# Performance work log

Hardware: AMD Instinct MI355X
Metric: run time of the kernel (lower is better)

Reference implementation:

```python
import jax, jax.numpy as jnp
import numpy as np

N_E = 16384
E_DIM = 256
SRC_DIM = 1024
BETA = 0.25


def setup_inputs() -> dict:
    key = jax.random.key(0)
    k_x, k_ew, k_eb, k_cb, k_dw, k_db = jax.random.split(key, 6)
    x = jax.random.normal(k_x, (16, 576, SRC_DIM), dtype=jnp.float32)
    # encoder Linear(source_dim -> embed_dim)
    enc_w = jax.random.normal(k_ew, (SRC_DIM, E_DIM), dtype=jnp.float32) / np.sqrt(SRC_DIM)
    enc_b = jax.random.normal(k_eb, (E_DIM,), dtype=jnp.float32) * 0.01
    # codebook initialized uniform(-1/n_e, 1/n_e) as in the torch module
    codebook = jax.random.uniform(k_cb, (N_E, E_DIM), dtype=jnp.float32, minval=-1.0 / N_E, maxval=1.0 / N_E)
    # decoder Linear(embed_dim -> source_dim)
    dec_w = jax.random.normal(k_dw, (E_DIM, SRC_DIM), dtype=jnp.float32) / np.sqrt(E_DIM)
    dec_b = jax.random.normal(k_db, (SRC_DIM,), dtype=jnp.float32) * 0.01
    return {"x": x, "enc_w": enc_w, "enc_b": enc_b, "codebook": codebook, "dec_w": dec_w, "dec_b": dec_b}


def reference(x, enc_w, enc_b, codebook, dec_w, dec_b):
    # encode: [B,S,src] -> [B,S,e]
    z = jnp.einsum('bsd,de->bse', x, enc_w) + enc_b
    # squared distances to all codebook entries: ||z||^2 + ||E||^2 - 2 z.E^T
    z2 = jnp.sum(z * z, axis=-1, keepdims=True)            # [B,S,1]
    e2 = jnp.sum(codebook * codebook, axis=-1)             # [n_e]
    cross = jnp.einsum('bse,ne->bsn', z, codebook)         # [B,S,n_e]
    d = z2 + e2 - 2.0 * cross
    idx = jnp.argmin(d, axis=-1)                           # [B,S] int
    z_q = codebook[idx]                                    # [B,S,e]
    sg = jax.lax.stop_gradient
    loss = BETA * jnp.mean((sg(z_q) - z) ** 2) + jnp.mean((z_q - sg(z)) ** 2)
    z_q_st = z + sg(z_q - z)                               # straight-through
    out = jnp.einsum('bse,ed->bsd', z_q_st, dec_w) + dec_b
    return (out, loss)
```

## Files before the change

kernel.cpp:

```cpp
#include <hip/hip_runtime.h>

typedef __bf16 bf16;
typedef __bf16 bf16x8 __attribute__((ext_vector_type(8)));
typedef float f32x4 __attribute__((ext_vector_type(4)));
typedef int i32x8 __attribute__((ext_vector_type(8)));
typedef unsigned int u32;
typedef unsigned char u8;

#define N_TOK 9216
#define SRC 1024
#define EDIM 256
#define NE 16384
#define GROUPS 16
#define GSIZE 1024
#define NBLK_GATHER 2304
#define NEG_CB_SCALE -8192.0f
#define E2_SCALE 4096.0f
#define LOSS_DENOM 2359296.0f

__device__ __forceinline__ void async_load16(const void* g, void* l) {
  __builtin_amdgcn_global_load_lds(
      (__attribute__((address_space(1))) void*)(void*)(const_cast<void*>(g)),
      (__attribute__((address_space(3))) void*)l, 16, 0, 0);
}

__device__ __forceinline__ f32x4 mfma16(bf16x8 a, bf16x8 b, f32x4 c) {
  return __builtin_amdgcn_mfma_f32_16x16x32_bf16(a, b, c, 0, 0, 0);
}
__device__ __forceinline__ f32x4 mfma_mx(i32x8 a, i32x8 b, f32x4 c) {
  return __builtin_amdgcn_mfma_scale_f32_16x16x128_f8f6f4(
      a, b, c, 0, 0, 0, 0x7F7F7F7F, 0, 0x7F7F7F7F);
}

__global__ __launch_bounds__(256) void k_prep(const float* __restrict__ enc_w,
                                              const float* __restrict__ dec_w,
                                              const float* __restrict__ cb,
                                              bf16* __restrict__ enc_wT,
                                              bf16* __restrict__ dec_wT,
                                              u32* __restrict__ cbb8,
                                              float* __restrict__ e2s) {
  int b = blockIdx.x;
  if (b < 1024) {
    int id = b * 256 + threadIdx.x;
    {
      int n = id >> 10, k = id & 1023;
      enc_wT[id] = (bf16)enc_w[k * EDIM + n];
    }
    {
      int n = id >> 8, k = id & 255;
      dec_wT[id] = (bf16)dec_w[k * SRC + n];
    }
  } else {
    int row = (b - 1024) * 4 + (threadIdx.x >> 6);
    int lane = threadIdx.x & 63;
    int slot = lane >> 2;
    int h = (slot & 8) | ((slot & 7) ^ (row & 7));
    int k0 = h * 16 + (lane & 3) * 4;
    float4 v = *(const float4*)(cb + (size_t)row * EDIM + k0);
    int pk = __builtin_amdgcn_cvt_pk_fp8_f32(v.x * NEG_CB_SCALE, v.y * NEG_CB_SCALE, 0, false);
    pk = __builtin_amdgcn_cvt_pk_fp8_f32(v.z * NEG_CB_SCALE, v.w * NEG_CB_SCALE, pk, true);
    cbb8[(size_t)row * 64 + lane] = (u32)pk;
    float sq = v.x * v.x + v.y * v.y + v.z * v.z + v.w * v.w;
#pragma unroll
    for (int off = 32; off; off >>= 1) sq += __shfl_xor(sq, off, 64);
    if (lane == 0) e2s[row] = E2_SCALE * (sq + 1.0f);
  }
}

__global__ __launch_bounds__(256) void k_enc(const float* __restrict__ x,
                                             const bf16* __restrict__ wT,
                                             const float* __restrict__ bias,
                                             u8* __restrict__ z8) {
  __shared__ __align__(16) bf16 As[2][64 * 32];
  __shared__ __align__(16) bf16 Bs[2][128 * 32];
  const int tid = threadIdx.x;
  const int wid = tid >> 6, lane = tid & 63;
  const int col = lane & 15, quad = lane >> 4;
  const int wm = (wid >> 1) * 32, wn = (wid & 1) * 64;
  const int bm = blockIdx.x * 64, bn = blockIdx.y * 128;
  f32x4 acc[2][4] = {};
  const int arow = tid >> 2, ags = tid & 3;

  float4 q0, q1;
  auto loadA = [&](int kc) {
    const float* p = x + (size_t)(bm + arow) * SRC + kc + ags * 8;
    q0 = *(const float4*)p;
    q1 = *(const float4*)(p + 4);
  };
  auto writeA = [&](int bb) {
    bf16x8 o = {(bf16)q0.x, (bf16)q0.y, (bf16)q0.z, (bf16)q0.w,
                (bf16)q1.x, (bf16)q1.y, (bf16)q1.z, (bf16)q1.w};
    *(bf16x8*)((char*)&As[bb][0] + (arow * 4 + (ags ^ (arow & 3))) * 16) = o;
  };
  auto stageB = [&](int kc, int bb) {
#pragma unroll
    for (int j = 0; j < 2; j++) {
      int slot = wid * 128 + j * 64 + lane;
      int row = slot >> 2;
      int gg = (slot & 3) ^ (row & 3);
      async_load16(wT + (size_t)(bn + row) * SRC + kc + gg * 8,
                   (char*)&Bs[bb][0] + wid * 2048 + j * 1024);
    }
  };

  loadA(0);
  writeA(0);
  stageB(0, 0);
  for (int it = 0; it < 32; it++) {
    int cbuf = it & 1, nbuf = cbuf ^ 1;
    if (it < 31) loadA((it + 1) * 32);
    __syncthreads();
    if (it < 31) stageB((it + 1) * 32, nbuf);
    bf16x8 afr[2], bfr[4];
#pragma unroll
    for (int t = 0; t < 2; t++) {
      int row = wm + t * 16 + col;
      afr[t] = *(const bf16x8*)((const char*)&As[cbuf][0] +
                                (row * 4 + (quad ^ (row & 3))) * 16);
    }
#pragma unroll
    for (int u = 0; u < 4; u++) {
      int row = wn + u * 16 + col;
      bfr[u] = *(const bf16x8*)((const char*)&Bs[cbuf][0] +
                                (row * 4 + (quad ^ (row & 3))) * 16);
    }
#pragma unroll
    for (int t = 0; t < 2; t++)
#pragma unroll
      for (int u = 0; u < 4; u++) acc[t][u] = mfma16(afr[t], bfr[u], acc[t][u]);
    if (it < 31) writeA(nbuf);
  }
#pragma unroll
  for (int u = 0; u < 4; u++) {
    int n = bn + wn + u * 16 + col;
    float bv = bias[n];
#pragma unroll
    for (int t = 0; t < 2; t++)
#pragma unroll
      for (int r = 0; r < 4; r++) {
        int m = bm + wm + t * 16 + quad * 4 + r;
        float v = acc[t][u][r] + bv;
        int pk = __builtin_amdgcn_cvt_pk_fp8_f32(v, v, 0, false);
        z8[(size_t)m * EDIM + n] = (u8)(pk & 0xFF);
      }
  }
}

__global__ __launch_bounds__(256, 3) void k_argmin(const u8* __restrict__ zb8,
                                                   const u8* __restrict__ cbb8,
                                                   const float* __restrict__ e2s,
                                                   float* __restrict__ pval,
                                                   int* __restrict__ pidx) {
  __shared__ __align__(16) u8 Cs[2 * 16384];
  const int tid = threadIdx.x;
  const int wid = tid >> 6, lane = tid & 63;
  const int col = lane & 15, quad = lane >> 4;
  const int g = blockIdx.y;
  const int tw = blockIdx.x * 192 + wid * 48;

  i32x8 af[3][2];
#pragma unroll
  for (int t = 0; t < 3; t++)
#pragma unroll
    for (int m = 0; m < 2; m++) {
      const u8* p = zb8 + (size_t)(tw + t * 16 + col) * EDIM + m * 128 + quad * 32;
      int4 lo = *(const int4*)p;
      int4 hi = *(const int4*)(p + 16);
      af[t][m] = (i32x8){lo.x, lo.y, lo.z, lo.w, hi.x, hi.y, hi.z, hi.w};
    }

  u32 best[3][4];
#pragma unroll
  for (int t = 0; t < 3; t++)
#pragma unroll
    for (int r = 0; r < 4; r++) best[t][r] = 0xFFFFFFFFu;

  auto stage_load = [&](int st, int bb) {
    const u8* src = cbb8 + (size_t)(g * GSIZE + st * 64) * EDIM;
#pragma unroll
    for (int j = 0; j < 4; j++) {
      async_load16(src + (wid * 256 + j * 64 + lane) * 16,
                   (char*)Cs + bb * 16384 + wid * 4096 + j * 1024);
    }
  };

  auto compute = [&](int st, int bb) {
    const char* bbase = (const char*)Cs + bb * 16384;
    const int cb0 = g * GSIZE + st * 64;
    float ev[4];
#pragma unroll
    for (int u = 0; u < 4; u++) ev[u] = e2s[cb0 + u * 16 + col];
    f32x4 c[3][4] = {};
    const int r7 = col & 7;
#pragma unroll
    for (int m = 0; m < 2; m++) {
#pragma unroll
      for (int u = 0; u < 4; u++) {
        int row = u * 16 + col;
        int s0 = m * 8 + ((2 * quad) ^ r7);
        int s1 = m * 8 + ((2 * quad + 1) ^ r7);
        int4 b0 = *(const int4*)(bbase + row * 256 + s0 * 16);
        int4 b1 = *(const int4*)(bbase + row * 256 + s1 * 16);
        i32x8 bfr = (i32x8){b0.x, b0.y, b0.z, b0.w, b1.x, b1.y, b1.z, b1.w};
#pragma unroll
        for (int t = 0; t < 3; t++) c[t][u] = mfma_mx(af[t][m], bfr, c[t][u]);
      }
    }
#pragma unroll
    for (int u = 0; u < 4; u++) {
      u32 iv = (u32)(st * 4 + u);
#pragma unroll
      for (int t = 0; t < 3; t++)
#pragma unroll
        for (int r = 0; r < 4; r++) {
          u32 du = __float_as_uint(c[t][u][r] + ev[u]);
          u32 key = (du & 0xFFFFFFC0u) | iv;
          best[t][r] = key < best[t][r] ? key : best[t][r];
        }
    }
  };

  stage_load(0, 0);
  for (int st = 0; st < 16; st++) {
    __syncthreads();
    if (st < 15) stage_load(st + 1, (st + 1) & 1);
    compute(st, st & 1);
  }

#pragma unroll
  for (int t = 0; t < 3; t++)
#pragma unroll
    for (int r = 0; r < 4; r++) {
      u32 key = best[t][r];
      int cw = col;
#pragma unroll
      for (int off = 1; off < 16; off <<= 1) {
        u32 ok = (u32)__shfl_xor((int)key, off, 64);
        int oc = __shfl_xor(cw, off, 64);
        if (ok < key) { key = ok; cw = oc; }
      }
      if (col == 0) {
        int token = tw + t * 16 + quad * 4 + r;
        pval[token * GROUPS + g] = __uint_as_float(key & 0xFFFFFFC0u);
        pidx[token * GROUPS + g] = g * GSIZE + (int)(key & 63u) * 16 + cw;
      }
    }
}

__global__ __launch_bounds__(256) void k_gather(const float* __restrict__ cb,
                                                const u8* __restrict__ zb8,
                                                const float* __restrict__ pval,
                                                const int* __restrict__ pidx,
                                                bf16* __restrict__ zqb,
                                                float* __restrict__ lpart) {
  __shared__ float ls[4];
  int wv = threadIdx.x >> 6;
  int token = blockIdx.x * 4 + wv;
  int lane = threadIdx.x & 63;
  float v = 3.4e38f;
  int idx = 0;
  if (lane < 16) {
    v = pval[token * GROUPS + lane];
    idx = pidx[token * GROUPS + lane];
  }
#pragma unroll
  for (int off = 1; off < 16; off <<= 1) {
    float ov = __shfl_xor(v, off, 64);
    int oi = __shfl_xor(idx, off, 64);
    if (ov < v || (ov == v && oi < idx)) { v = ov; idx = oi; }
  }
  idx = __shfl(idx, 0, 64);
  float4 q = ((const float4*)(cb + (size_t)idx * EDIM))[lane];
  u32 zw = *(const u32*)(zb8 + (size_t)token * EDIM + lane * 4);
  float z0 = __builtin_amdgcn_cvt_f32_fp8(zw, 0);
  float z1 = __builtin_amdgcn_cvt_f32_fp8(zw, 1);
  float z2 = __builtin_amdgcn_cvt_f32_fp8(zw, 2);
  float z3 = __builtin_amdgcn_cvt_f32_fp8(zw, 3);
  bf16* zq = zqb + (size_t)token * EDIM + lane * 4;
  zq[0] = (bf16)q.x;
  zq[1] = (bf16)q.y;
  zq[2] = (bf16)q.z;
  zq[3] = (bf16)q.w;
  float dx = q.x - z0, dy = q.y - z1, dz = q.z - z2, dw = q.w - z3;
  float s = dx * dx + dy * dy + dz * dz + dw * dw;
#pragma unroll
  for (int off = 32; off; off >>= 1) s += __shfl_xor(s, off, 64);
  if (lane == 0) ls[wv] = s;
  __syncthreads();
  if (threadIdx.x == 0) lpart[blockIdx.x] = ls[0] + ls[1] + ls[2] + ls[3];
}

__global__ __launch_bounds__(256) void k_dec(const bf16* __restrict__ A,
                                             const bf16* __restrict__ wT,
                                             const float* __restrict__ bias,
                                             float* __restrict__ out) {
  __shared__ __align__(16) bf16 As[2][64 * 32];
  __shared__ __align__(16) bf16 Bs[2][256 * 32];
  const int tid = threadIdx.x;
  const int wid = tid >> 6, lane = tid & 63;
  const int col = lane & 15, quad = lane >> 4;
  const int wm = (wid >> 1) * 32, wn = (wid & 1) * 128;
  const int bm = blockIdx.x * 64, bn = blockIdx.y * 256;
  f32x4 acc[2][8] = {};

  auto stageA = [&](int kc, int bb) {
    int slot = wid * 64 + lane;
    int row = slot >> 2;
    int gg = (slot & 3) ^ (row & 3);
    async_load16(A + (size_t)(bm + row) * EDIM + kc + gg * 8,
                 (char*)&As[bb][0] + wid * 1024);
  };
  auto stageB = [&](int kc, int bb) {
#pragma unroll
    for (int j = 0; j < 4; j++) {
      int slot = wid * 256 + j * 64 + lane;
      int row = slot >> 2;
      int gg = (slot & 3) ^ (row & 3);
      async_load16(wT + (size_t)(bn + row) * EDIM + kc + gg * 8,
                   (char*)&Bs[bb][0] + wid * 4096 + j * 1024);
    }
  };

  stageA(0, 0);
  stageB(0, 0);
  for (int it = 0; it < 8; it++) {
    int cbuf = it & 1, nbuf = cbuf ^ 1;
    __syncthreads();
    if (it < 7) {
      stageA((it + 1) * 32, nbuf);
      stageB((it + 1) * 32, nbuf);
    }
    bf16x8 afr[2], bfr[8];
#pragma unroll
    for (int t = 0; t < 2; t++) {
      int row = wm + t * 16 + col;
      afr[t] = *(const bf16x8*)((const char*)&As[cbuf][0] +
                                (row * 4 + (quad ^ (row & 3))) * 16);
    }
#pragma unroll
    for (int u = 0; u < 8; u++) {
      int row = wn + u * 16 + col;
      bfr[u] = *(const bf16x8*)((const char*)&Bs[cbuf][0] +
                                (row * 4 + (quad ^ (row & 3))) * 16);
    }
#pragma unroll
    for (int t = 0; t < 2; t++)
#pragma unroll
      for (int u = 0; u < 8; u++) acc[t][u] = mfma16(afr[t], bfr[u], acc[t][u]);
  }
#pragma unroll
  for (int u = 0; u < 8; u++) {
    int n = bn + wn + u * 16 + col;
    float bv = bias[n];
#pragma unroll
    for (int t = 0; t < 2; t++)
#pragma unroll
      for (int r = 0; r < 4; r++) {
        int m = bm + wm + t * 16 + quad * 4 + r;
        out[(size_t)m * SRC + n] = acc[t][u][r] + bv;
      }
  }
}

__global__ __launch_bounds__(256) void k_loss(const float* __restrict__ lpart,
                                              float* __restrict__ outl) {
  __shared__ float ls[4];
  float s = 0.f;
  for (int i = threadIdx.x; i < NBLK_GATHER; i += 256) s += lpart[i];
#pragma unroll
  for (int off = 32; off; off >>= 1) s += __shfl_xor(s, off, 64);
  int wv = threadIdx.x >> 6;
  if ((threadIdx.x & 63) == 0) ls[wv] = s;
  __syncthreads();
  if (threadIdx.x == 0) *outl = 1.25f * (ls[0] + ls[1] + ls[2] + ls[3]) / LOSS_DENOM;
}

extern "C" void kernel_launch(void* const* d_in, const int* in_sizes, int n_in,
                              void* d_out, int out_size, void* d_ws, size_t ws_size,
                              hipStream_t stream) {
  const float* x = (const float*)d_in[0];
  const float* enc_w = (const float*)d_in[1];
  const float* enc_b = (const float*)d_in[2];
  const float* cb = (const float*)d_in[3];
  const float* dec_w = (const float*)d_in[4];
  const float* dec_b = (const float*)d_in[5];
  float* out = (float*)d_out;
  float* out_loss = out + (size_t)N_TOK * SRC;

  char* ws = (char*)d_ws;
  bf16* enc_wT = (bf16*)(ws + 0);
  bf16* dec_wT = (bf16*)(ws + 524288);
  u8* zb8 = (u8*)(ws + 1048576);
  u32* cbb8 = (u32*)(ws + 3407872);
  float* e2s = (float*)(ws + 7602176);
  float* pval = (float*)(ws + 7667712);
  int* pidx = (int*)(ws + 8257536);
  bf16* zqb = (bf16*)(ws + 8847360);
  float* lpart = (float*)(ws + 13565952);

  k_prep<<<5120, 256, 0, stream>>>(enc_w, dec_w, cb, enc_wT, dec_wT, cbb8, e2s);
  k_enc<<<dim3(144, 2), 256, 0, stream>>>(x, enc_wT, enc_b, zb8);
  k_argmin<<<dim3(48, GROUPS), 256, 0, stream>>>(zb8, (const u8*)cbb8, e2s, pval, pidx);
  k_gather<<<NBLK_GATHER, 256, 0, stream>>>(cb, zb8, pval, pidx, zqb, lpart);
  k_dec<<<dim3(144, 4), 256, 0, stream>>>(zqb, dec_wT, dec_b, out);
  k_loss<<<1, 256, 0, stream>>>(lpart, out_loss);
}
```

Baseline: 199.9 us.

## Fuse gather into decoder, tile weight transposes, retile encoder, cache e2 in LDS

Removes the separate gather kernel: the decoder now reduces the per-group argmin partials itself, loads the selected codebook rows directly as its A operand, and computes the commitment loss in its blockIdx.y==0 blocks. This drops the intermediate bf16 z_q buffer round trip and one launch, and shrinks the loss reduction input. The prep kernel uses LDS-tiled transposes for the weights instead of strided scalar reads. The encoder switches to 64x64 tiles for more blocks. The argmin kernel stages e2 in LDS, folds it into the accumulator init, and uses a min-tree for the key comparison. The gathered A rows are now read with plain loads rather than async copies, which could stall the decoder pipeline.

```diff
diff --git a/kernel.cpp b/kernel.cpp
--- a/kernel.cpp
+++ b/kernel.cpp
@@ -13,7 +13,7 @@
 #define NE 16384
 #define GROUPS 16
 #define GSIZE 1024
-#define NBLK_GATHER 2304
+#define NBLK_LOSS 144
 #define NEG_CB_SCALE -8192.0f
 #define E2_SCALE 4096.0f
 #define LOSS_DENOM 2359296.0f
@@ -40,18 +40,33 @@
                                               u32* __restrict__ cbb8,
                                               float* __restrict__ e2s) {
   int b = blockIdx.x;
-  if (b < 1024) {
-    int id = b * 256 + threadIdx.x;
-    {
-      int n = id >> 10, k = id & 1023;
-      enc_wT[id] = (bf16)enc_w[k * EDIM + n];
-    }
-    {
-      int n = id >> 8, k = id & 255;
-      dec_wT[id] = (bf16)dec_w[k * SRC + n];
+  if (b < 128) {
+    __shared__ float T[64][65];
+    const float* In;
+    bf16* Out;
+    int R, C, ti, tj;
+    if (b < 64) {
+      In = enc_w; Out = enc_wT; R = 1024; C = 256;
+      ti = b & 15; tj = b >> 4;
+    } else {
+      int t2 = b - 64;
+      In = dec_w; Out = dec_wT; R = 256; C = 1024;
+      ti = t2 & 3; tj = t2 >> 2;
+    }
+    int c0 = threadIdx.x & 63, r0 = threadIdx.x >> 6;
+#pragma unroll
+    for (int i = 0; i < 16; i++) {
+      int rr = r0 + i * 4;
+      T[rr][c0] = In[(size_t)(ti * 64 + rr) * C + tj * 64 + c0];
+    }
+    __syncthreads();
+#pragma unroll
+    for (int i = 0; i < 16; i++) {
+      int rr = r0 + i * 4;
+      Out[(size_t)(tj * 64 + rr) * R + ti * 64 + c0] = (bf16)T[c0][rr];
     }
   } else {
-    int row = (b - 1024) * 4 + (threadIdx.x >> 6);
+    int row = (b - 128) * 4 + (threadIdx.x >> 6);
     int lane = threadIdx.x & 63;
     int slot = lane >> 2;
     int h = (slot & 8) | ((slot & 7) ^ (row & 7));
@@ -72,13 +87,13 @@
                                              const float* __restrict__ bias,
                                              u8* __restrict__ z8) {
   __shared__ __align__(16) bf16 As[2][64 * 32];
-  __shared__ __align__(16) bf16 Bs[2][128 * 32];
+  __shared__ __align__(16) bf16 Bs[2][64 * 32];
   const int tid = threadIdx.x;
   const int wid = tid >> 6, lane = tid & 63;
   const int col = lane & 15, quad = lane >> 4;
-  const int wm = (wid >> 1) * 32, wn = (wid & 1) * 64;
-  const int bm = blockIdx.x * 64, bn = blockIdx.y * 128;
-  f32x4 acc[2][4] = {};
+  const int wm = (wid >> 1) * 32, wn = (wid & 1) * 32;
+  const int bm = blockIdx.x * 64, bn = blockIdx.y * 64;
+  f32x4 acc[2][2] = {};
   const int arow = tid >> 2, ags = tid & 3;
 
   float4 q0, q1;
@@ -93,14 +108,10 @@
     *(bf16x8*)((char*)&As[bb][0] + (arow * 4 + (ags ^ (arow & 3))) * 16) = o;
   };
   auto stageB = [&](int kc, int bb) {
-#pragma unroll
-    for (int j = 0; j < 2; j++) {
-      int slot = wid * 128 + j * 64 + lane;
-      int row = slot >> 2;
-      int gg = (slot & 3) ^ (row & 3);
-      async_load16(wT + (size_t)(bn + row) * SRC + kc + gg * 8,
-                   (char*)&Bs[bb][0] + wid * 2048 + j * 1024);
-    }
+    int row = tid >> 2;
+    int gg = (tid & 3) ^ (row & 3);
+    async_load16(wT + (size_t)(bn + row) * SRC + kc + gg * 8,
+                 (char*)&Bs[bb][0] + wid * 1024);
   };
 
   loadA(0);
@@ -108,10 +119,12 @@
   stageB(0, 0);
   for (int it = 0; it < 32; it++) {
     int cbuf = it & 1, nbuf = cbuf ^ 1;
-    if (it < 31) loadA((it + 1) * 32);
     __syncthreads();
-    if (it < 31) stageB((it + 1) * 32, nbuf);
-    bf16x8 afr[2], bfr[4];
+    if (it < 31) {
+      loadA((it + 1) * 32);
+      stageB((it + 1) * 32, nbuf);
+    }
+    bf16x8 afr[2], bfr[2];
 #pragma unroll
     for (int t = 0; t < 2; t++) {
       int row = wm + t * 16 + col;
@@ -119,7 +132,7 @@
                                 (row * 4 + (quad ^ (row & 3))) * 16);
     }
 #pragma unroll
-    for (int u = 0; u < 4; u++) {
+    for (int u = 0; u < 2; u++) {
       int row = wn + u * 16 + col;
       bfr[u] = *(const bf16x8*)((const char*)&Bs[cbuf][0] +
                                 (row * 4 + (quad ^ (row & 3))) * 16);
@@ -127,11 +140,11 @@
 #pragma unroll
     for (int t = 0; t < 2; t++)
 #pragma unroll
-      for (int u = 0; u < 4; u++) acc[t][u] = mfma16(afr[t], bfr[u], acc[t][u]);
+      for (int u = 0; u < 2; u++) acc[t][u] = mfma16(afr[t], bfr[u], acc[t][u]);
     if (it < 31) writeA(nbuf);
   }
 #pragma unroll
-  for (int u = 0; u < 4; u++) {
+  for (int u = 0; u < 2; u++) {
     int n = bn + wn + u * 16 + col;
     float bv = bias[n];
 #pragma unroll
@@ -152,12 +165,16 @@
                                                    float* __restrict__ pval,
                                                    int* __restrict__ pidx) {
   __shared__ __align__(16) u8 Cs[2 * 16384];
+  __shared__ __align__(16) float Es[1024];
   const int tid = threadIdx.x;
   const int wid = tid >> 6, lane = tid & 63;
   const int col = lane & 15, quad = lane >> 4;
   const int g = blockIdx.y;
   const int tw = blockIdx.x * 192 + wid * 48;
 
+  async_load16((const u8*)(e2s + g * GSIZE) + (size_t)tid * 16,
+               (char*)Es + wid * 1024);
+
   i32x8 af[3][2];
 #pragma unroll
   for (int t = 0; t < 3; t++)
@@ -186,11 +203,15 @@
 
   auto compute = [&](int st, int bb) {
     const char* bbase = (const char*)Cs + bb * 16384;
-    const int cb0 = g * GSIZE + st * 64;
     float ev[4];
 #pragma unroll
-    for (int u = 0; u < 4; u++) ev[u] = e2s[cb0 + u * 16 + col];
-    f32x4 c[3][4] = {};
+    for (int u = 0; u < 4; u++) ev[u] = Es[st * 64 + u * 16 + col];
+    f32x4 c[3][4];
+#pragma unroll
+    for (int t = 0; t < 3; t++)
+#pragma unroll
+      for (int u = 0; u < 4; u++)
+        c[t][u] = (f32x4){ev[u], ev[u], ev[u], ev[u]};
     const int r7 = col & 7;
 #pragma unroll
     for (int m = 0; m < 2; m++) {
@@ -207,17 +228,18 @@
       }
     }
 #pragma unroll
-    for (int u = 0; u < 4; u++) {
-      u32 iv = (u32)(st * 4 + u);
-#pragma unroll
-      for (int t = 0; t < 3; t++)
-#pragma unroll
-        for (int r = 0; r < 4; r++) {
-          u32 du = __float_as_uint(c[t][u][r] + ev[u]);
-          u32 key = (du & 0xFFFFFFC0u) | iv;
-          best[t][r] = key < best[t][r] ? key : best[t][r];
-        }
-    }
+    for (int t = 0; t < 3; t++)
+#pragma unroll
+      for (int r = 0; r < 4; r++) {
+        u32 k0 = (__float_as_uint(c[t][0][r]) & 0xFFFFFFC0u) | (u32)(st * 4 + 0);
+        u32 k1 = (__float_as_uint(c[t][1][r]) & 0xFFFFFFC0u) | (u32)(st * 4 + 1);
+        u32 k2 = (__float_as_uint(c[t][2][r]) & 0xFFFFFFC0u) | (u32)(st * 4 + 2);
+        u32 k3 = (__float_as_uint(c[t][3][r]) & 0xFFFFFFC0u) | (u32)(st * 4 + 3);
+        u32 a = k0 < k1 ? k0 : k1;
+        u32 bm_ = k2 < k3 ? k2 : k3;
+        u32 m_ = a < bm_ ? a : bm_;
+        best[t][r] = m_ < best[t][r] ? m_ : best[t][r];
+      }
   };
 
   stage_load(0, 0);
@@ -247,68 +269,75 @@
     }
 }
 
-__global__ __launch_bounds__(256) void k_gather(const float* __restrict__ cb,
-                                                const u8* __restrict__ zb8,
-                                                const float* __restrict__ pval,
-                                                const int* __restrict__ pidx,
-                                                bf16* __restrict__ zqb,
-                                                float* __restrict__ lpart) {
-  __shared__ float ls[4];
-  int wv = threadIdx.x >> 6;
-  int token = blockIdx.x * 4 + wv;
-  int lane = threadIdx.x & 63;
-  float v = 3.4e38f;
-  int idx = 0;
-  if (lane < 16) {
-    v = pval[token * GROUPS + lane];
-    idx = pidx[token * GROUPS + lane];
-  }
-#pragma unroll
-  for (int off = 1; off < 16; off <<= 1) {
-    float ov = __shfl_xor(v, off, 64);
-    int oi = __shfl_xor(idx, off, 64);
-    if (ov < v || (ov == v && oi < idx)) { v = ov; idx = oi; }
-  }
-  idx = __shfl(idx, 0, 64);
-  float4 q = ((const float4*)(cb + (size_t)idx * EDIM))[lane];
-  u32 zw = *(const u32*)(zb8 + (size_t)token * EDIM + lane * 4);
-  float z0 = __builtin_amdgcn_cvt_f32_fp8(zw, 0);
-  float z1 = __builtin_amdgcn_cvt_f32_fp8(zw, 1);
-  float z2 = __builtin_amdgcn_cvt_f32_fp8(zw, 2);
-  float z3 = __builtin_amdgcn_cvt_f32_fp8(zw, 3);
-  bf16* zq = zqb + (size_t)token * EDIM + lane * 4;
-  zq[0] = (bf16)q.x;
-  zq[1] = (bf16)q.y;
-  zq[2] = (bf16)q.z;
-  zq[3] = (bf16)q.w;
-  float dx = q.x - z0, dy = q.y - z1, dz = q.z - z2, dw = q.w - z3;
-  float s = dx * dx + dy * dy + dz * dz + dw * dw;
-#pragma unroll
-  for (int off = 32; off; off >>= 1) s += __shfl_xor(s, off, 64);
-  if (lane == 0) ls[wv] = s;
-  __syncthreads();
-  if (threadIdx.x == 0) lpart[blockIdx.x] = ls[0] + ls[1] + ls[2] + ls[3];
-}
-
-__global__ __launch_bounds__(256) void k_dec(const bf16* __restrict__ A,
+__global__ __launch_bounds__(256) void k_dec(const float* __restrict__ cb,
+                                             const float* __restrict__ pval,
+                                             const int* __restrict__ pidx,
+                                             const u8* __restrict__ zb8,
                                              const bf16* __restrict__ wT,
                                              const float* __restrict__ bias,
-                                             float* __restrict__ out) {
+                                             float* __restrict__ out,
+                                             float* __restrict__ lpart) {
   __shared__ __align__(16) bf16 As[2][64 * 32];
   __shared__ __align__(16) bf16 Bs[2][256 * 32];
+  __shared__ int idxL[64];
+  __shared__ float lsred[4];
   const int tid = threadIdx.x;
   const int wid = tid >> 6, lane = tid & 63;
   const int col = lane & 15, quad = lane >> 4;
   const int wm = (wid >> 1) * 32, wn = (wid & 1) * 128;
   const int bm = blockIdx.x * 64, bn = blockIdx.y * 256;
+  const bool do_loss = (blockIdx.y == 0);
+
+  {
+    int tl = tid >> 2, j0 = tid & 3;
+    float v = 3.4e38f;
+    int idx = 0;
+#pragma unroll
+    for (int jj = 0; jj < 4; jj++) {
+      int grp = j0 * 4 + jj;
+      float ov = pval[(bm + tl) * GROUPS + grp];
+      int oi = pidx[(bm + tl) * GROUPS + grp];
+      if (ov < v || (ov == v && oi < idx)) { v = ov; idx = oi; }
+    }
+#pragma unroll
+    for (int off = 1; off < 4; off <<= 1) {
+      float ov = __shfl_xor(v, off, 64);
+      int oi = __shfl_xor(idx, off, 64);
+      if (ov < v || (ov == v && oi < idx)) { v = ov; idx = oi; }
+    }
+    if (j0 == 0) idxL[tl] = idx;
+  }
+  __syncthreads();
+
+  const int arow = tid >> 2, ags = tid & 3;
+  const int ridx = idxL[arow];
+  float lacc = 0.f;
   f32x4 acc[2][8] = {};
 
-  auto stageA = [&](int kc, int bb) {
-    int slot = wid * 64 + lane;
-    int row = slot >> 2;
-    int gg = (slot & 3) ^ (row & 3);
-    async_load16(A + (size_t)(bm + row) * EDIM + kc + gg * 8,
-                 (char*)&As[bb][0] + wid * 1024);
+  float4 q0, q1;
+  auto loadA = [&](int kc) {
+    const float* p = cb + (size_t)ridx * EDIM + kc + ags * 8;
+    q0 = *(const float4*)p;
+    q1 = *(const float4*)(p + 4);
+    if (do_loss) {
+      u32 zw0 = *(const u32*)(zb8 + (size_t)(bm + arow) * EDIM + kc + ags * 8);
+      u32 zw1 = *(const u32*)(zb8 + (size_t)(bm + arow) * EDIM + kc + ags * 8 + 4);
+      float d0 = q0.x - __builtin_amdgcn_cvt_f32_fp8(zw0, 0);
+      float d1 = q0.y - __builtin_amdgcn_cvt_f32_fp8(zw0, 1);
+      float d2 = q0.z - __builtin_amdgcn_cvt_f32_fp8(zw0, 2);
+      float d3 = q0.w - __builtin_amdgcn_cvt_f32_fp8(zw0, 3);
+      float d4 = q1.x - __builtin_amdgcn_cvt_f32_fp8(zw1, 0);
+      float d5 = q1.y - __builtin_amdgcn_cvt_f32_fp8(zw1, 1);
+      float d6 = q1.z - __builtin_amdgcn_cvt_f32_fp8(zw1, 2);
+      float d7 = q1.w - __builtin_amdgcn_cvt_f32_fp8(zw1, 3);
+      lacc += d0 * d0 + d1 * d1 + d2 * d2 + d3 * d3 +
+              d4 * d4 + d5 * d5 + d6 * d6 + d7 * d7;
+    }
+  };
+  auto writeA = [&](int bb) {
+    bf16x8 o = {(bf16)q0.x, (bf16)q0.y, (bf16)q0.z, (bf16)q0.w,
+                (bf16)q1.x, (bf16)q1.y, (bf16)q1.z, (bf16)q1.w};
+    *(bf16x8*)((char*)&As[bb][0] + (arow * 4 + (ags ^ (arow & 3))) * 16) = o;
   };
   auto stageB = [&](int kc, int bb) {
 #pragma unroll
@@ -321,13 +350,14 @@
     }
   };
 
-  stageA(0, 0);
+  loadA(0);
+  writeA(0);
   stageB(0, 0);
   for (int it = 0; it < 8; it++) {
     int cbuf = it & 1, nbuf = cbuf ^ 1;
     __syncthreads();
     if (it < 7) {
-      stageA((it + 1) * 32, nbuf);
+      loadA((it + 1) * 32);
       stageB((it + 1) * 32, nbuf);
     }
     bf16x8 afr[2], bfr[8];
@@ -347,7 +377,9 @@
     for (int t = 0; t < 2; t++)
 #pragma unroll
       for (int u = 0; u < 8; u++) acc[t][u] = mfma16(afr[t], bfr[u], acc[t][u]);
-  }
+    if (it < 7) writeA(nbuf);
+  }
+
 #pragma unroll
   for (int u = 0; u < 8; u++) {
     int n = bn + wn + u * 16 + col;
@@ -360,15 +392,23 @@
         out[(size_t)m * SRC + n] = acc[t][u][r] + bv;
       }
   }
+
+  if (do_loss) {
+#pragma unroll
+    for (int off = 32; off; off >>= 1) lacc += __shfl_xor(lacc, off, 64);
+    if (lane == 0) lsred[wid] = lacc;
+    __syncthreads();
+    if (tid == 0) lpart[blockIdx.x] = lsred[0] + lsred[1] + lsred[2] + lsred[3];
+  }
 }
 
 __global__ __launch_bounds__(256) void k_loss(const float* __restrict__ lpart,
                                               float* __restrict__ outl) {
+  float s = 0.f;
+  if (threadIdx.x < NBLK_LOSS) s = lpart[threadIdx.x];
+#pragma unroll
+  for (int off = 32; off; off >>= 1) s += __shfl_xor(s, off, 64);
   __shared__ float ls[4];
-  float s = 0.f;
-  for (int i = threadIdx.x; i < NBLK_GATHER; i += 256) s += lpart[i];
-#pragma unroll
-  for (int off = 32; off; off >>= 1) s += __shfl_xor(s, off, 64);
   int wv = threadIdx.x >> 6;
   if ((threadIdx.x & 63) == 0) ls[wv] = s;
   __syncthreads();
@@ -395,13 +435,11 @@
   float* e2s = (float*)(ws + 7602176);
   float* pval = (float*)(ws + 7667712);
   int* pidx = (int*)(ws + 8257536);
-  bf16* zqb = (bf16*)(ws + 8847360);
-  float* lpart = (float*)(ws + 13565952);
-
-  k_prep<<<5120, 256, 0, stream>>>(enc_w, dec_w, cb, enc_wT, dec_wT, cbb8, e2s);
-  k_enc<<<dim3(144, 2), 256, 0, stream>>>(x, enc_wT, enc_b, zb8);
+  float* lpart = (float*)(ws + 8847360);
+
+  k_prep<<<4224, 256, 0, stream>>>(enc_w, dec_w, cb, enc_wT, dec_wT, cbb8, e2s);
+  k_enc<<<dim3(144, 4), 256, 0, stream>>>(x, enc_wT, enc_b, zb8);
   k_argmin<<<dim3(48, GROUPS), 256, 0, stream>>>(zb8, (const u8*)cbb8, e2s, pval, pidx);
-  k_gather<<<NBLK_GATHER, 256, 0, stream>>>(cb, zb8, pval, pidx, zqb, lpart);
-  k_dec<<<dim3(144, 4), 256, 0, stream>>>(zqb, dec_wT, dec_b, out);
+  k_dec<<<dim3(144, 4), 256, 0, stream>>>(cb, pval, pidx, zb8, dec_wT, dec_b, out, lpart);
   k_loss<<<1, 256, 0, stream>>>(lpart, out_loss);
 }
```

Result: faster. 189.5 us (-5.2%).
